# Performance work log

Hardware: AMD Instinct MI355X
Metric: run time of the kernel (lower is better)

## Reference

```python
import jax, jax.numpy as jnp
import numpy as np

N_DOMAINS = 8
LN_EPS = 1e-5


def setup_inputs() -> dict:
    key = jax.random.key(0)
    ks = jax.random.split(key, 4)
    N, D_IN, D_HID, D_OUT = 32768, 256, 1024, 256
    x = jax.random.normal(ks[0], (N, D_IN), dtype=jnp.float32)
    domain_types = jax.random.randint(ks[1], (N,), 0, N_DOMAINS, dtype=jnp.int32)
    # Per-domain MLP parameters (8 independent experts)
    W1 = jax.random.normal(ks[2], (N_DOMAINS, D_IN, D_HID), dtype=jnp.float32) * (1.0 / np.sqrt(D_IN))
    b1 = jnp.zeros((N_DOMAINS, D_HID), dtype=jnp.float32)
    gamma = jnp.ones((N_DOMAINS, D_HID), dtype=jnp.float32)
    beta = jnp.zeros((N_DOMAINS, D_HID), dtype=jnp.float32)
    W2 = jax.random.normal(ks[3], (N_DOMAINS, D_HID, D_OUT), dtype=jnp.float32) * (1.0 / np.sqrt(D_HID))
    b2 = jnp.zeros((N_DOMAINS, D_OUT), dtype=jnp.float32)
    return {"x": x, "domain_types": domain_types, "W1": W1, "b1": b1,
            "gamma": gamma, "beta": beta, "W2": W2, "b2": b2}


def _expert_mlp(x, W1d, b1d, gd, bd, W2d, b2d):
    # Linear -> LayerNorm -> ReLU -> (Dropout: identity at eval) -> Linear
    h = x @ W1d + b1d                       # [N, hid]
    mu = jnp.mean(h, axis=-1, keepdims=True)
    var = jnp.mean(jnp.square(h - mu), axis=-1, keepdims=True)
    h = (h - mu) * jax.lax.rsqrt(var + LN_EPS) * gd + bd
    h = jax.nn.relu(h)
    return h @ W2d + b2d                    # [N, out]


def reference(x, domain_types, W1, b1, gamma, beta, W2, b2):
    # output dim == x.shape[-1] (as in the torch code: zeros(batch, x.shape[-1]))
    out = jnp.zeros((x.shape[0], x.shape[-1]), dtype=x.dtype)
    for d in range(N_DOMAINS):  # small fixed expert loop (static MoE dispatch)
        y = _expert_mlp(x, W1[d], b1[d], gamma[d], beta[d], W2[d], b2[d])
        mask = (domain_types == d)[:, None]
        out = jnp.where(mask, y, out)
    return out
```

## Files before the change

kernel.cpp:

```cpp
#include <hip/hip_runtime.h>
#include <hip/hip_bf16.h>


#define ND 8
#define NROWS 32768
#define DIN 256
#define DHID 1024
#define DOUT 256
#define MPAD 33792
#define NTILES 264

typedef short short8 __attribute__((ext_vector_type(8)));
typedef unsigned short ushort8v __attribute__((ext_vector_type(8)));
typedef float floatx4 __attribute__((ext_vector_type(4)));

__device__ __forceinline__ unsigned short f2bf(float f) {
    unsigned u = __builtin_bit_cast(unsigned, f);
    unsigned r = u + 0x7fff + ((u >> 16) & 1);
    return (unsigned short)(r >> 16);
}
__device__ __forceinline__ float bf2f(unsigned short h) {
    unsigned u = ((unsigned)h) << 16;
    return __builtin_bit_cast(float, u);
}

#define GLDS16(gp, lp) __builtin_amdgcn_global_load_lds( \
    (const __attribute__((address_space(1))) void*)(gp), \
    (__attribute__((address_space(3))) void*)(lp), 16, 0, 0)

__global__ void transpose_bf16(const float* __restrict__ in,
                               unsigned short* __restrict__ out,
                               int R, int C, int* __restrict__ cnt) {
    __shared__ float t[32][33];
    const int z = blockIdx.z;
    const int c0 = blockIdx.x * 32, r0 = blockIdx.y * 32;
    const int tx = threadIdx.x & 31, ty = threadIdx.x >> 5;
    if (cnt && blockIdx.x == 0 && blockIdx.y == 0 && z == 0 && threadIdx.x < 16)
        cnt[threadIdx.x] = 0;
    const float* src = in + (size_t)z * R * C;
    unsigned short* dst = out + (size_t)z * R * C;
#pragma unroll
    for (int i = 0; i < 32; i += 8)
        t[ty + i][tx] = src[(size_t)(r0 + ty + i) * C + c0 + tx];
    __syncthreads();
#pragma unroll
    for (int i = 0; i < 32; i += 8)
        dst[(size_t)(c0 + ty + i) * R + r0 + tx] = f2bf(t[tx][ty + i]);
}

__global__ void histo(const int* __restrict__ dt, int* __restrict__ counts) {
    __shared__ int lc[ND];
    if (threadIdx.x < ND) lc[threadIdx.x] = 0;
    __syncthreads();
    int i = blockIdx.x * 256 + threadIdx.x;
    atomicAdd(&lc[dt[i]], 1);
    __syncthreads();
    if (threadIdx.x < ND) atomicAdd(&counts[threadIdx.x], lc[threadIdx.x]);
}

__global__ void make_meta(const int* __restrict__ counts, int* __restrict__ cursors,
                          int2* __restrict__ meta, int* __restrict__ perm) {
    if (threadIdx.x == 0 && blockIdx.x == 0) {
        int off = 0, t = 0;
        for (int d = 0; d < ND; d++) {
            cursors[d] = off;
            int nt = (counts[d] + 127) >> 7;
            for (int i = 0; i < nt; i++) meta[t++] = make_int2(d, off + (i << 7));
            for (int p = off + counts[d]; p < off + (nt << 7); p++) perm[p] = -1;
            off += nt << 7;
        }
        for (; t < NTILES; t++) meta[t] = make_int2(-1, 0);
    }
}

__global__ __launch_bounds__(256)
void assign_pos(const int* __restrict__ dt, int* __restrict__ cursors,
                int* __restrict__ perm, int* __restrict__ pos) {
    __shared__ int lcnt[ND];
    __shared__ int lbase[ND];
    const int tid = threadIdx.x;
    if (tid < ND) lcnt[tid] = 0;
    __syncthreads();
    const int r = blockIdx.x * 256 + tid;
    const int d = dt[r];
    const int myrank = atomicAdd(&lcnt[d], 1);
    __syncthreads();
    if (tid < ND && lcnt[tid] > 0)
        lbase[tid] = atomicAdd(&cursors[tid], lcnt[tid]);
    __syncthreads();
    const int p = lbase[d] + myrank;
    pos[r] = p;
    perm[p] = r;
}

__global__ __launch_bounds__(256)
void copy_rows(const float* __restrict__ x, const int* __restrict__ pos,
               unsigned short* __restrict__ xs) {
    const int tid = threadIdx.x;
    const int lane = tid & 63;
    const int r = blockIdx.x * 4 + (tid >> 6);
    const int p = pos[r];
    float4 v = ((const float4*)(x + (size_t)r * DIN))[lane];
    ushort4 o;
    o.x = f2bf(v.x); o.y = f2bf(v.y); o.z = f2bf(v.z); o.w = f2bf(v.w);
    ((ushort4*)(xs + (size_t)p * DIN))[lane] = o;
}

__global__ __launch_bounds__(256, 2)
void gemm_a(const unsigned short* __restrict__ A,
            const unsigned short* __restrict__ Bt,
            const float* __restrict__ bias,
            const int2* __restrict__ meta,
            unsigned short* __restrict__ H,
            float2* __restrict__ stats) {
    const int2 md = meta[blockIdx.x];
    const int dom = md.x;
    if (dom < 0) return;
    const int m0 = md.y;
    const int n0 = blockIdx.y * 128;

    __shared__ unsigned short As[128 * 32];
    __shared__ unsigned short Bs[128 * 32];

    const int tid = threadIdx.x;
    const int lane = tid & 63;
    const int w = tid >> 6;
    const int wr = w >> 1, wc = w & 1;
    const int c16 = lane & 15, quad = lane >> 4;

    const unsigned short* Abase = A + (size_t)m0 * DIN;
    const unsigned short* Bbase = Bt + (size_t)dom * DHID * DIN + (size_t)n0 * DIN;

    floatx4 acc[4][4];
#pragma unroll
    for (int i = 0; i < 4; i++)
#pragma unroll
        for (int j = 0; j < 4; j++) acc[i][j] = 0.f;

    for (int k0 = 0; k0 < DIN; k0 += 32) {
#pragma unroll
        for (int it = 0; it < 2; ++it) {
            const int c = w * 128 + it * 64 + lane;
            const int m = c >> 2, kc = c & 3;
            GLDS16(Abase + (size_t)m * DIN + k0 + kc * 8, &As[(w * 128 + it * 64) * 8]);
            GLDS16(Bbase + (size_t)m * DIN + k0 + kc * 8, &Bs[(w * 128 + it * 64) * 8]);
        }
        __syncthreads();

        short8 a[4], b[4];
        const int kk = quad * 8;
#pragma unroll
        for (int i = 0; i < 4; i++) {
            a[i] = *(const short8*)&As[(wr * 64 + i * 16 + c16) * 32 + kk];
            b[i] = *(const short8*)&Bs[(wc * 64 + i * 16 + c16) * 32 + kk];
        }
#pragma unroll
        for (int i = 0; i < 4; i++)
#pragma unroll
            for (int j = 0; j < 4; j++)
                acc[i][j] = __builtin_amdgcn_mfma_f32_16x16x32_bf16(a[i], b[j], acc[i][j], 0, 0, 0);
        __syncthreads();
    }

    float bv[4];
#pragma unroll
    for (int j = 0; j < 4; j++)
        bv[j] = bias[dom * DHID + n0 + wc * 64 + j * 16 + c16];

    float2* st = stats + (size_t)(blockIdx.y * 2 + wc) * MPAD;
#pragma unroll
    for (int i = 0; i < 4; i++) {
        const int rowbase = m0 + wr * 64 + i * 16 + quad * 4;
#pragma unroll
        for (int r = 0; r < 4; r++) {
            float s = 0.f, q = 0.f;
#pragma unroll
            for (int j = 0; j < 4; j++) {
                const float v = acc[i][j][r] + bv[j];
                const int col = n0 + wc * 64 + j * 16 + c16;
                H[(size_t)(rowbase + r) * DHID + col] = f2bf(v);
                s += v; q += v * v;
            }
#pragma unroll
            for (int o = 1; o < 16; o <<= 1) {
                s += __shfl_xor(s, o, 64);
                q += __shfl_xor(q, o, 64);
            }
            if (c16 == 0) st[rowbase + r] = make_float2(s, q);
        }
    }
}

__global__ __launch_bounds__(256, 2)
void gemm_b_ln(const unsigned short* __restrict__ H,
               const unsigned short* __restrict__ Bt,
               const float* __restrict__ bias,
               const float* __restrict__ gamma,
               const float* __restrict__ beta,
               const float2* __restrict__ stats,
               const int2* __restrict__ meta,
               const int* __restrict__ perm,
               float* __restrict__ out) {
    const int2 md = meta[blockIdx.x];
    const int dom = md.x;
    if (dom < 0) return;
    const int m0 = md.y;
    const int n0 = blockIdx.y * 128;

    __shared__ unsigned short As[128 * 32];
    __shared__ unsigned short Bs[128 * 32];
    __shared__ float mu_s[128], rs_s[128];

    const int tid = threadIdx.x;
    const int lane = tid & 63;
    const int w = tid >> 6;
    const int wr = w >> 1, wc = w & 1;
    const int c16 = lane & 15, quad = lane >> 4;

    if (tid < 128) {
        float s = 0.f, q = 0.f;
#pragma unroll
        for (int cb = 0; cb < 16; cb++) {
            const float2 p = stats[(size_t)cb * MPAD + m0 + tid];
            s += p.x; q += p.y;
        }
        const float inv = 1.0f / (float)DHID;
        const float mu = s * inv;
        const float var = fmaxf(q * inv - mu * mu, 0.f);
        mu_s[tid] = mu;
        rs_s[tid] = rsqrtf(var + 1e-5f);
    }
    __syncthreads();

    const unsigned short* Hbase = H + (size_t)m0 * DHID;
    const unsigned short* Bbase = Bt + (size_t)dom * DOUT * DHID + (size_t)n0 * DHID;
    const float* gbase = gamma + dom * DHID;
    const float* bbase = beta + dom * DHID;

    floatx4 acc[4][4];
#pragma unroll
    for (int i = 0; i < 4; i++)
#pragma unroll
        for (int j = 0; j < 4; j++) acc[i][j] = 0.f;

    for (int k0 = 0; k0 < DHID; k0 += 32) {
#pragma unroll
        for (int it = 0; it < 2; ++it) {
            const int c = it * 256 + tid;
            const int row = c >> 2, kg = c & 3;
            const float mu = mu_s[row], rs = rs_s[row];
            const ushort8v hv = *(const ushort8v*)(Hbase + (size_t)row * DHID + k0 + kg * 8);
            const float4 g0 = *(const float4*)(gbase + k0 + kg * 8);
            const float4 g1 = *(const float4*)(gbase + k0 + kg * 8 + 4);
            const float4 b0 = *(const float4*)(bbase + k0 + kg * 8);
            const float4 b1 = *(const float4*)(bbase + k0 + kg * 8 + 4);
            float gg[8] = {g0.x, g0.y, g0.z, g0.w, g1.x, g1.y, g1.z, g1.w};
            float bb[8] = {b0.x, b0.y, b0.z, b0.w, b1.x, b1.y, b1.z, b1.w};
            ushort8v o;
#pragma unroll
            for (int e = 0; e < 8; e++) {
                const float v = (bf2f(hv[e]) - mu) * rs;
                o[e] = f2bf(fmaxf(v * gg[e] + bb[e], 0.f));
            }
            *(ushort8v*)&As[row * 32 + kg * 8] = o;
        }
#pragma unroll
        for (int it = 0; it < 2; ++it) {
            const int c = w * 128 + it * 64 + lane;
            const int m = c >> 2, kc = c & 3;
            GLDS16(Bbase + (size_t)m * DHID + k0 + kc * 8, &Bs[(w * 128 + it * 64) * 8]);
        }
        __syncthreads();

        short8 a[4], b[4];
        const int kk = quad * 8;
#pragma unroll
        for (int i = 0; i < 4; i++) {
            a[i] = *(const short8*)&As[(wr * 64 + i * 16 + c16) * 32 + kk];
            b[i] = *(const short8*)&Bs[(wc * 64 + i * 16 + c16) * 32 + kk];
        }
#pragma unroll
        for (int i = 0; i < 4; i++)
#pragma unroll
            for (int j = 0; j < 4; j++)
                acc[i][j] = __builtin_amdgcn_mfma_f32_16x16x32_bf16(a[i], b[j], acc[i][j], 0, 0, 0);
        __syncthreads();
    }

#pragma unroll
    for (int i = 0; i < 4; i++) {
        const int rowbase = m0 + wr * 64 + i * 16 + quad * 4;
#pragma unroll
        for (int r = 0; r < 4; r++) {
            const int orig = perm[rowbase + r];
            if (orig < 0) continue;
#pragma unroll
            for (int j = 0; j < 4; j++) {
                const int col = n0 + wc * 64 + j * 16 + c16;
                out[(size_t)orig * DOUT + col] = acc[i][j][r] + bias[dom * DOUT + col];
            }
        }
    }
}

extern "C" void kernel_launch(void* const* d_in, const int* in_sizes, int n_in,
                              void* d_out, int out_size, void* d_ws, size_t ws_size,
                              hipStream_t stream) {
    const float* x = (const float*)d_in[0];
    const int* dt = (const int*)d_in[1];
    const float* W1 = (const float*)d_in[2];
    const float* b1 = (const float*)d_in[3];
    const float* gamma = (const float*)d_in[4];
    const float* beta = (const float*)d_in[5];
    const float* W2 = (const float*)d_in[6];
    const float* b2 = (const float*)d_in[7];
    float* out = (float*)d_out;

    char* ws = (char*)d_ws;
    size_t off = 0;
    auto take = [&](size_t nbytes) -> char* {
        char* p = ws + off;
        off = (off + nbytes + 255) & ~(size_t)255;
        return p;
    };
    unsigned short* W1T = (unsigned short*)take((size_t)ND * DHID * DIN * 2);
    unsigned short* W2T = (unsigned short*)take((size_t)ND * DOUT * DHID * 2);
    unsigned short* XS  = (unsigned short*)take((size_t)MPAD * DIN * 2);
    unsigned short* H   = (unsigned short*)take((size_t)MPAD * DHID * 2);
    float2* STATS = (float2*)take((size_t)16 * MPAD * 8);
    int* PERM   = (int*)take(MPAD * 4);
    int* POS    = (int*)take(NROWS * 4);
    int* CNT    = (int*)take(64);
    int2* META  = (int2*)take(NTILES * 8);
    (void)ws_size; (void)n_in; (void)in_sizes; (void)out_size;

    int* COUNTS = CNT;
    int* CURSORS = CNT + 8;

    transpose_bf16<<<dim3(DHID / 32, DIN / 32, ND), 256, 0, stream>>>(W1, W1T, DIN, DHID, CNT);
    transpose_bf16<<<dim3(DOUT / 32, DHID / 32, ND), 256, 0, stream>>>(W2, W2T, DHID, DOUT, nullptr);
    histo<<<NROWS / 256, 256, 0, stream>>>(dt, COUNTS);
    make_meta<<<1, 1, 0, stream>>>(COUNTS, CURSORS, META, PERM);
    assign_pos<<<NROWS / 256, 256, 0, stream>>>(dt, CURSORS, PERM, POS);
    copy_rows<<<NROWS / 4, 256, 0, stream>>>(x, POS, XS);
    gemm_a<<<dim3(NTILES, DHID / 128), 256, 0, stream>>>(XS, W1T, b1, META, H, STATS);
    gemm_b_ln<<<dim3(NTILES, DOUT / 128), 256, 0, stream>>>(
        H, W2T, b2, gamma, beta, STATS, META, PERM, out);
}
```

Measured before the change: 229.2 us.

## Widen GEMM tiles to 128x256, merge weight transposes, prefetch H in LN GEMM

```diff
diff --git a/kernel.cpp b/kernel.cpp
--- a/kernel.cpp
+++ b/kernel.cpp
@@ -28,17 +28,24 @@
     (const __attribute__((address_space(1))) void*)(gp), \
     (__attribute__((address_space(3))) void*)(lp), 16, 0, 0)
 
-__global__ void transpose_bf16(const float* __restrict__ in,
-                               unsigned short* __restrict__ out,
-                               int R, int C, int* __restrict__ cnt) {
+__global__ void transpose_both(const float* __restrict__ W1,
+                               const float* __restrict__ W2,
+                               unsigned short* __restrict__ W1T,
+                               unsigned short* __restrict__ W2T,
+                               int* __restrict__ cnt) {
     __shared__ float t[32][33];
     const int z = blockIdx.z;
-    const int c0 = blockIdx.x * 32, r0 = blockIdx.y * 32;
+    const bool isW1 = z < ND;
+    const int d = isW1 ? z : z - ND;
+    const int R = isW1 ? DIN : DHID;
+    const int C = isW1 ? DHID : DOUT;
+    const int r0 = (isW1 ? blockIdx.x : blockIdx.y) * 32;
+    const int c0 = (isW1 ? blockIdx.y : blockIdx.x) * 32;
     const int tx = threadIdx.x & 31, ty = threadIdx.x >> 5;
-    if (cnt && blockIdx.x == 0 && blockIdx.y == 0 && z == 0 && threadIdx.x < 16)
+    if (z == 0 && blockIdx.x == 0 && blockIdx.y == 0 && threadIdx.x < 16)
         cnt[threadIdx.x] = 0;
-    const float* src = in + (size_t)z * R * C;
-    unsigned short* dst = out + (size_t)z * R * C;
+    const float* src = (isW1 ? W1 : W2) + (size_t)d * R * C;
+    unsigned short* dst = (isW1 ? W1T : W2T) + (size_t)d * R * C;
 #pragma unroll
     for (int i = 0; i < 32; i += 8)
         t[ty + i][tx] = src[(size_t)(r0 + ty + i) * C + c0 + tx];
@@ -60,17 +67,23 @@
 
 __global__ void make_meta(const int* __restrict__ counts, int* __restrict__ cursors,
                           int2* __restrict__ meta, int* __restrict__ perm) {
-    if (threadIdx.x == 0 && blockIdx.x == 0) {
+    __shared__ int ps[ND], pe[ND];
+    if (threadIdx.x == 0) {
         int off = 0, t = 0;
         for (int d = 0; d < ND; d++) {
             cursors[d] = off;
             int nt = (counts[d] + 127) >> 7;
             for (int i = 0; i < nt; i++) meta[t++] = make_int2(d, off + (i << 7));
-            for (int p = off + counts[d]; p < off + (nt << 7); p++) perm[p] = -1;
+            ps[d] = off + counts[d];
+            pe[d] = off + (nt << 7);
             off += nt << 7;
         }
         for (; t < NTILES; t++) meta[t] = make_int2(-1, 0);
     }
+    __syncthreads();
+#pragma unroll
+    for (int d = 0; d < ND; d++)
+        for (int p = ps[d] + threadIdx.x; p < pe[d]; p += 256) perm[p] = -1;
 }
 
 __global__ __launch_bounds__(256)
@@ -117,10 +130,10 @@
     const int dom = md.x;
     if (dom < 0) return;
     const int m0 = md.y;
-    const int n0 = blockIdx.y * 128;
+    const int n0 = blockIdx.y * 256;
 
     __shared__ unsigned short As[128 * 32];
-    __shared__ unsigned short Bs[128 * 32];
+    __shared__ unsigned short Bs[256 * 32];
 
     const int tid = threadIdx.x;
     const int lane = tid & 63;
@@ -131,11 +144,11 @@
     const unsigned short* Abase = A + (size_t)m0 * DIN;
     const unsigned short* Bbase = Bt + (size_t)dom * DHID * DIN + (size_t)n0 * DIN;
 
-    floatx4 acc[4][4];
+    floatx4 acc[4][8];
 #pragma unroll
     for (int i = 0; i < 4; i++)
 #pragma unroll
-        for (int j = 0; j < 4; j++) acc[i][j] = 0.f;
+        for (int j = 0; j < 8; j++) acc[i][j] = 0.f;
 
     for (int k0 = 0; k0 < DIN; k0 += 32) {
 #pragma unroll
@@ -143,29 +156,35 @@
             const int c = w * 128 + it * 64 + lane;
             const int m = c >> 2, kc = c & 3;
             GLDS16(Abase + (size_t)m * DIN + k0 + kc * 8, &As[(w * 128 + it * 64) * 8]);
-            GLDS16(Bbase + (size_t)m * DIN + k0 + kc * 8, &Bs[(w * 128 + it * 64) * 8]);
+        }
+#pragma unroll
+        for (int it = 0; it < 4; ++it) {
+            const int c = w * 256 + it * 64 + lane;
+            const int n = c >> 2, kc = c & 3;
+            GLDS16(Bbase + (size_t)n * DIN + k0 + kc * 8, &Bs[(w * 256 + it * 64) * 8]);
         }
         __syncthreads();
 
-        short8 a[4], b[4];
+        short8 a[4], b[8];
         const int kk = quad * 8;
 #pragma unroll
-        for (int i = 0; i < 4; i++) {
+        for (int i = 0; i < 4; i++)
             a[i] = *(const short8*)&As[(wr * 64 + i * 16 + c16) * 32 + kk];
-            b[i] = *(const short8*)&Bs[(wc * 64 + i * 16 + c16) * 32 + kk];
-        }
+#pragma unroll
+        for (int j = 0; j < 8; j++)
+            b[j] = *(const short8*)&Bs[(wc * 128 + j * 16 + c16) * 32 + kk];
 #pragma unroll
         for (int i = 0; i < 4; i++)
 #pragma unroll
-            for (int j = 0; j < 4; j++)
+            for (int j = 0; j < 8; j++)
                 acc[i][j] = __builtin_amdgcn_mfma_f32_16x16x32_bf16(a[i], b[j], acc[i][j], 0, 0, 0);
         __syncthreads();
     }
 
-    float bv[4];
-#pragma unroll
-    for (int j = 0; j < 4; j++)
-        bv[j] = bias[dom * DHID + n0 + wc * 64 + j * 16 + c16];
+    float bv[8];
+#pragma unroll
+    for (int j = 0; j < 8; j++)
+        bv[j] = bias[dom * DHID + n0 + wc * 128 + j * 16 + c16];
 
     float2* st = stats + (size_t)(blockIdx.y * 2 + wc) * MPAD;
 #pragma unroll
@@ -174,11 +193,11 @@
 #pragma unroll
         for (int r = 0; r < 4; r++) {
             float s = 0.f, q = 0.f;
-#pragma unroll
-            for (int j = 0; j < 4; j++) {
+            unsigned short* hrow = H + (size_t)(rowbase + r) * DHID + n0 + wc * 128;
+#pragma unroll
+            for (int j = 0; j < 8; j++) {
                 const float v = acc[i][j][r] + bv[j];
-                const int col = n0 + wc * 64 + j * 16 + c16;
-                H[(size_t)(rowbase + r) * DHID + col] = f2bf(v);
+                hrow[j * 16 + c16] = f2bf(v);
                 s += v; q += v * v;
             }
 #pragma unroll
@@ -191,7 +210,7 @@
     }
 }
 
-__global__ __launch_bounds__(256, 2)
+__global__ __launch_bounds__(256, 1)
 void gemm_b_ln(const unsigned short* __restrict__ H,
                const unsigned short* __restrict__ Bt,
                const float* __restrict__ bias,
@@ -205,10 +224,11 @@
     const int dom = md.x;
     if (dom < 0) return;
     const int m0 = md.y;
-    const int n0 = blockIdx.y * 128;
 
     __shared__ unsigned short As[128 * 32];
-    __shared__ unsigned short Bs[128 * 32];
+    __shared__ unsigned short Bs[256 * 32];
+    __shared__ unsigned short gsh[DHID];
+    __shared__ unsigned short bsh[DHID];
     __shared__ float mu_s[128], rs_s[128];
 
     const int tid = threadIdx.x;
@@ -220,7 +240,7 @@
     if (tid < 128) {
         float s = 0.f, q = 0.f;
 #pragma unroll
-        for (int cb = 0; cb < 16; cb++) {
+        for (int cb = 0; cb < 8; cb++) {
             const float2 p = stats[(size_t)cb * MPAD + m0 + tid];
             s += p.x; q += p.y;
         }
@@ -230,63 +250,83 @@
         mu_s[tid] = mu;
         rs_s[tid] = rsqrtf(var + 1e-5f);
     }
+    {
+        const int base = tid * 4;
+        const float4 g4 = *(const float4*)(gamma + dom * DHID + base);
+        const float4 b4 = *(const float4*)(beta + dom * DHID + base);
+        gsh[base + 0] = f2bf(g4.x); gsh[base + 1] = f2bf(g4.y);
+        gsh[base + 2] = f2bf(g4.z); gsh[base + 3] = f2bf(g4.w);
+        bsh[base + 0] = f2bf(b4.x); bsh[base + 1] = f2bf(b4.y);
+        bsh[base + 2] = f2bf(b4.z); bsh[base + 3] = f2bf(b4.w);
+    }
     __syncthreads();
 
     const unsigned short* Hbase = H + (size_t)m0 * DHID;
-    const unsigned short* Bbase = Bt + (size_t)dom * DOUT * DHID + (size_t)n0 * DHID;
-    const float* gbase = gamma + dom * DHID;
-    const float* bbase = beta + dom * DHID;
-
-    floatx4 acc[4][4];
+    const unsigned short* Bbase = Bt + (size_t)dom * DOUT * DHID;
+
+    floatx4 acc[4][8];
 #pragma unroll
     for (int i = 0; i < 4; i++)
 #pragma unroll
-        for (int j = 0; j < 4; j++) acc[i][j] = 0.f;
+        for (int j = 0; j < 8; j++) acc[i][j] = 0.f;
+
+    const int c0i = tid, c1i = 256 + tid;
+    const int row0 = c0i >> 2, kg0 = c0i & 3;
+    const int row1 = c1i >> 2, kg1 = c1i & 3;
+    ushort8v hv0 = *(const ushort8v*)(Hbase + (size_t)row0 * DHID + kg0 * 8);
+    ushort8v hv1 = *(const ushort8v*)(Hbase + (size_t)row1 * DHID + kg1 * 8);
 
     for (int k0 = 0; k0 < DHID; k0 += 32) {
-#pragma unroll
-        for (int it = 0; it < 2; ++it) {
-            const int c = it * 256 + tid;
-            const int row = c >> 2, kg = c & 3;
-            const float mu = mu_s[row], rs = rs_s[row];
-            const ushort8v hv = *(const ushort8v*)(Hbase + (size_t)row * DHID + k0 + kg * 8);
-            const float4 g0 = *(const float4*)(gbase + k0 + kg * 8);
-            const float4 g1 = *(const float4*)(gbase + k0 + kg * 8 + 4);
-            const float4 b0 = *(const float4*)(bbase + k0 + kg * 8);
-            const float4 b1 = *(const float4*)(bbase + k0 + kg * 8 + 4);
-            float gg[8] = {g0.x, g0.y, g0.z, g0.w, g1.x, g1.y, g1.z, g1.w};
-            float bb[8] = {b0.x, b0.y, b0.z, b0.w, b1.x, b1.y, b1.z, b1.w};
-            ushort8v o;
+        {
+            const float mu0 = mu_s[row0], rs0 = rs_s[row0];
+            const float mu1 = mu_s[row1], rs1 = rs_s[row1];
+            const ushort8v g0 = *(const ushort8v*)&gsh[k0 + kg0 * 8];
+            const ushort8v b0 = *(const ushort8v*)&bsh[k0 + kg0 * 8];
+            const ushort8v g1 = *(const ushort8v*)&gsh[k0 + kg1 * 8];
+            const ushort8v b1v = *(const ushort8v*)&bsh[k0 + kg1 * 8];
+            ushort8v o0, o1;
 #pragma unroll
             for (int e = 0; e < 8; e++) {
-                const float v = (bf2f(hv[e]) - mu) * rs;
-                o[e] = f2bf(fmaxf(v * gg[e] + bb[e], 0.f));
+                const float t0 = (bf2f(hv0[e]) - mu0) * rs0;
+                o0[e] = f2bf(fmaxf(t0 * bf2f(g0[e]) + bf2f(b0[e]), 0.f));
+                const float t1 = (bf2f(hv1[e]) - mu1) * rs1;
+                o1[e] = f2bf(fmaxf(t1 * bf2f(g1[e]) + bf2f(b1v[e]), 0.f));
             }
-            *(ushort8v*)&As[row * 32 + kg * 8] = o;
-        }
-#pragma unroll
-        for (int it = 0; it < 2; ++it) {
-            const int c = w * 128 + it * 64 + lane;
-            const int m = c >> 2, kc = c & 3;
-            GLDS16(Bbase + (size_t)m * DHID + k0 + kc * 8, &Bs[(w * 128 + it * 64) * 8]);
+            *(ushort8v*)&As[row0 * 32 + kg0 * 8] = o0;
+            *(ushort8v*)&As[row1 * 32 + kg1 * 8] = o1;
+        }
+#pragma unroll
+        for (int it = 0; it < 4; ++it) {
+            const int c = w * 256 + it * 64 + lane;
+            const int n = c >> 2, kc = c & 3;
+            GLDS16(Bbase + (size_t)n * DHID + k0 + kc * 8, &Bs[(w * 256 + it * 64) * 8]);
+        }
+        if (k0 + 32 < DHID) {
+            hv0 = *(const ushort8v*)(Hbase + (size_t)row0 * DHID + k0 + 32 + kg0 * 8);
+            hv1 = *(const ushort8v*)(Hbase + (size_t)row1 * DHID + k0 + 32 + kg1 * 8);
         }
         __syncthreads();
 
-        short8 a[4], b[4];
+        short8 a[4], b[8];
         const int kk = quad * 8;
 #pragma unroll
-        for (int i = 0; i < 4; i++) {
+        for (int i = 0; i < 4; i++)
             a[i] = *(const short8*)&As[(wr * 64 + i * 16 + c16) * 32 + kk];
-            b[i] = *(const short8*)&Bs[(wc * 64 + i * 16 + c16) * 32 + kk];
-        }
+#pragma unroll
+        for (int j = 0; j < 8; j++)
+            b[j] = *(const short8*)&Bs[(wc * 128 + j * 16 + c16) * 32 + kk];
 #pragma unroll
         for (int i = 0; i < 4; i++)
 #pragma unroll
-            for (int j = 0; j < 4; j++)
+            for (int j = 0; j < 8; j++)
                 acc[i][j] = __builtin_amdgcn_mfma_f32_16x16x32_bf16(a[i], b[j], acc[i][j], 0, 0, 0);
         __syncthreads();
     }
 
+    float bv[8];
+#pragma unroll
+    for (int j = 0; j < 8; j++)
+        bv[j] = bias[dom * DOUT + wc * 128 + j * 16 + c16];
 #pragma unroll
     for (int i = 0; i < 4; i++) {
         const int rowbase = m0 + wr * 64 + i * 16 + quad * 4;
@@ -295,9 +335,9 @@
             const int orig = perm[rowbase + r];
             if (orig < 0) continue;
 #pragma unroll
-            for (int j = 0; j < 4; j++) {
-                const int col = n0 + wc * 64 + j * 16 + c16;
-                out[(size_t)orig * DOUT + col] = acc[i][j][r] + bias[dom * DOUT + col];
+            for (int j = 0; j < 8; j++) {
+                const int col = wc * 128 + j * 16 + c16;
+                out[(size_t)orig * DOUT + col] = acc[i][j][r] + bv[j];
             }
         }
     }
@@ -327,7 +367,7 @@
     unsigned short* W2T = (unsigned short*)take((size_t)ND * DOUT * DHID * 2);
     unsigned short* XS  = (unsigned short*)take((size_t)MPAD * DIN * 2);
     unsigned short* H   = (unsigned short*)take((size_t)MPAD * DHID * 2);
-    float2* STATS = (float2*)take((size_t)16 * MPAD * 8);
+    float2* STATS = (float2*)take((size_t)8 * MPAD * 8);
     int* PERM   = (int*)take(MPAD * 4);
     int* POS    = (int*)take(NROWS * 4);
     int* CNT    = (int*)take(64);
@@ -337,13 +377,12 @@
     int* COUNTS = CNT;
     int* CURSORS = CNT + 8;
 
-    transpose_bf16<<<dim3(DHID / 32, DIN / 32, ND), 256, 0, stream>>>(W1, W1T, DIN, DHID, CNT);
-    transpose_bf16<<<dim3(DOUT / 32, DHID / 32, ND), 256, 0, stream>>>(W2, W2T, DHID, DOUT, nullptr);
+    transpose_both<<<dim3(8, 32, 16), 256, 0, stream>>>(W1, W2, W1T, W2T, CNT);
     histo<<<NROWS / 256, 256, 0, stream>>>(dt, COUNTS);
-    make_meta<<<1, 1, 0, stream>>>(COUNTS, CURSORS, META, PERM);
+    make_meta<<<1, 256, 0, stream>>>(COUNTS, CURSORS, META, PERM);
     assign_pos<<<NROWS / 256, 256, 0, stream>>>(dt, CURSORS, PERM, POS);
     copy_rows<<<NROWS / 4, 256, 0, stream>>>(x, POS, XS);
-    gemm_a<<<dim3(NTILES, DHID / 128), 256, 0, stream>>>(XS, W1T, b1, META, H, STATS);
-    gemm_b_ln<<<dim3(NTILES, DOUT / 128), 256, 0, stream>>>(
+    gemm_a<<<dim3(NTILES, 4), 256, 0, stream>>>(XS, W1T, b1, META, H, STATS);
+    gemm_b_ln<<<NTILES, 256, 0, stream>>>(
         H, W2T, b2, gamma, beta, STATS, META, PERM, out);
 }
```

Measured after the change: 246.9 us. 1.08x slower.
